# Kernel optimization log

Measured on AMD Instinct MI355X. Metric: run time of the kernel, lower is better.

Reference implementation:

```python
import jax, jax.numpy as jnp
import numpy as np

HUGE = 1e8  # stand-in for ops.HUGE_INT

B, P, Q, PD, QD = 16, 1024, 512, 768, 768


def setup_inputs() -> dict:
    key = jax.random.key(0)
    k1, k2, k3, k4, k5 = jax.random.split(key, 5)
    p = jax.random.normal(k1, (B, P, PD), dtype=jnp.float32)
    q = jax.random.normal(k2, (B, Q, QD), dtype=jnp.float32)
    # True = padded position (masked out before softmax)
    p_masks = jax.random.randint(k3, (B, P), 0, 2).astype(bool)
    q_masks = jax.random.randint(k4, (B, Q), 0, 2).astype(bool)
    # projection weight of Linear(q_dim, p_dim, bias=False): [p_dim, q_dim]
    W = jax.random.normal(k5, (PD, QD), dtype=jnp.float32) / np.sqrt(QD)
    return {"p": p, "q": q, "p_masks": p_masks, "q_masks": q_masks, "W": W}


def reference(p, q, p_masks, q_masks, W):
    # q_proj = project(q): [B,Q,p_dim]; dropout=0.0 -> identity
    q_proj = jnp.einsum('bqd,pd->bqp', q, W)
    # affinity = p @ q_proj^T : [B,P,Q]
    affinity = jnp.einsum('bpd,bqd->bpq', p, q_proj)
    # normalize over dim 1 with padding mask broadcast over last dim
    attn_over_p = jax.nn.softmax(
        jnp.where(p_masks[:, :, None], -HUGE, affinity), axis=1)  # [B,P,Q]
    attn_over_q = jax.nn.softmax(
        jnp.where(q_masks[:, :, None], -HUGE, jnp.swapaxes(affinity, 1, 2)), axis=1)  # [B,Q,P]
    # attn(weights[B,W2,W3], cand[B,W2,C3]) -> [B,W3,C3] = weights^T @ cand
    q_to_p_attn_vec = jnp.einsum('bpq,bpd->bqd', attn_over_p, p)  # [B,Q,p_dim]
    cand = jnp.concatenate([q, q_to_p_attn_vec], axis=2)  # [B,Q,q_dim+p_dim]
    p_to_q_attn_vec = jnp.einsum('bqp,bqc->bpc', attn_over_q, cand)  # [B,P,q_dim+p_dim]
    return (p_to_q_attn_vec, q_to_p_attn_vec)
```

## Files before the change

### kernel.cpp

```cpp
#include <hip/hip_runtime.h>
#include <math.h>

constexpr int B_  = 16;
constexpr int P_  = 1024;
constexpr int Q_  = 512;
constexpr int PD_ = 768;
constexpr int QD_ = 768;
constexpr int CD_ = 1536;

#define HUGE_NEG (-1e8f)

typedef __attribute__((ext_vector_type(8))) _Float16 f16x8;
typedef __attribute__((ext_vector_type(4))) _Float16 f16x4;
typedef __attribute__((ext_vector_type(4))) float f32x4;

__device__ __forceinline__ void dma16(const void* g, void* l) {
  __builtin_amdgcn_global_load_lds((__attribute__((address_space(1))) void*)g,
                                   (__attribute__((address_space(3))) void*)l,
                                   16, 0, 0);
}

__global__ __launch_bounds__(256) void k_cvt(const float* __restrict__ src,
                                             _Float16* __restrict__ dst, int n8) {
  int i = blockIdx.x * 256 + threadIdx.x;
  if (i >= n8) return;
  float4 a = ((const float4*)src)[2 * i];
  float4 b = ((const float4*)src)[2 * i + 1];
  f16x8 o = {(_Float16)a.x, (_Float16)a.y, (_Float16)a.z, (_Float16)a.w,
             (_Float16)b.x, (_Float16)b.y, (_Float16)b.z, (_Float16)b.w};
  ((f16x8*)dst)[i] = o;
}

__global__ __launch_bounds__(256) void k_prep(const float* __restrict__ src,
                                              _Float16* __restrict__ dst16,
                                              _Float16* __restrict__ dstT,
                                              int R, int C, size_t tBatch) {
  __shared__ _Float16 T[64][72];
  int r0 = blockIdx.x * 64, c0 = blockIdx.y * 64, b = blockIdx.z;
  const float* S = src + (size_t)b * R * C;
  _Float16* D16 = dst16 + (size_t)b * R * C;
  int tid = threadIdx.x;
  int rr = tid >> 4;
  int cc = (tid & 15) * 4;
#pragma unroll
  for (int k = 0; k < 4; ++k) {
    int r = rr + k * 16;
    float4 v = *(const float4*)(S + (size_t)(r0 + r) * C + c0 + cc);
    f16x4 h = {(_Float16)v.x, (_Float16)v.y, (_Float16)v.z, (_Float16)v.w};
    *(f16x4*)(D16 + (size_t)(r0 + r) * C + c0 + cc) = h;
    T[cc + 0][r] = h[0];
    T[cc + 1][r] = h[1];
    T[cc + 2][r] = h[2];
    T[cc + 3][r] = h[3];
  }
  __syncthreads();
  int cr = tid >> 2;
  int rc = (tid & 3) * 16;
  _Float16* D = dstT + (size_t)b * tBatch + (size_t)(c0 + cr) * R + r0;
  *(f16x8*)(D + rc) = *(f16x8*)&T[cr][rc];
  *(f16x8*)(D + rc + 8) = *(f16x8*)&T[cr][rc + 8];
}

__global__ __launch_bounds__(256) void k_w(
    const float* __restrict__ aff, const int* __restrict__ pmask,
    const int* __restrict__ qmask, const float* __restrict__ rpm,
    const float* __restrict__ rps, const float* __restrict__ pmax_part,
    const float* __restrict__ psum_part, _Float16* __restrict__ WP,
    _Float16* __restrict__ WQ) {
  __shared__ _Float16 T[64][72];
  __shared__ float rmx[64], rin[64], cmx[64], cin[64];
  int p0 = blockIdx.x * 64, q0 = blockIdx.y * 64, b = blockIdx.z;
  int tid = threadIdx.x;
  if (tid < 64) {
    int pp = p0 + tid;
    float m = -INFINITY;
#pragma unroll
    for (int z = 0; z < 4; ++z) m = fmaxf(m, rpm[(b * 4 + z) * P_ + pp]);
    float s = 0.f;
#pragma unroll
    for (int z = 0; z < 4; ++z)
      s += rps[(b * 4 + z) * P_ + pp] * __expf(rpm[(b * 4 + z) * P_ + pp] - m);
    rmx[tid] = m;
    rin[tid] = 1.0f / s;
  } else if (tid < 128) {
    int t = tid - 64;
    int qq = q0 + t;
    float m = -INFINITY;
#pragma unroll
    for (int z = 0; z < 4; ++z) m = fmaxf(m, pmax_part[(b * 4 + z) * Q_ + qq]);
    float s = 0.f;
#pragma unroll
    for (int z = 0; z < 4; ++z)
      s += psum_part[(b * 4 + z) * Q_ + qq] *
           __expf(pmax_part[(b * 4 + z) * Q_ + qq] - m);
    cmx[t] = m;
    cin[t] = 1.0f / s;
  }
  __syncthreads();
  const float* A = aff + (size_t)b * P_ * Q_;
  const int* pm = pmask + b * P_;
  int rr = tid >> 4;
  int cc = (tid & 15) * 4;
  int4 qm4 = *(const int4*)(qmask + b * Q_ + q0 + cc);
  int qm[4] = {qm4.x, qm4.y, qm4.z, qm4.w};
#pragma unroll
  for (int k = 0; k < 4; ++k) {
    int r = rr + k * 16;
    int msk = pm[p0 + r];
    float4 v = *(const float4*)(A + (size_t)(p0 + r) * Q_ + q0 + cc);
    float vv[4] = {v.x, v.y, v.z, v.w};
    f16x4 wp;
#pragma unroll
    for (int j = 0; j < 4; ++j) {
      wp[j] = (_Float16)(__expf((qm[j] ? HUGE_NEG : vv[j]) - rmx[r]) * rin[r]);
      T[cc + j][r] =
          (_Float16)(__expf((msk ? HUGE_NEG : vv[j]) - cmx[cc + j]) * cin[cc + j]);
    }
    *(f16x4*)(WP + ((size_t)b * P_ + p0 + r) * Q_ + q0 + cc) = wp;
  }
  __syncthreads();
  int cr = tid >> 2;
  int rc = (tid & 3) * 16;
  _Float16* D = WQ + ((size_t)b * Q_ + q0 + cr) * P_ + p0;
  *(f16x8*)(D + rc) = *(f16x8*)&T[cr][rc];
  *(f16x8*)(D + rc + 8) = *(f16x8*)&T[cr][rc + 8];
}

template <int NT, int LDA, int LDB>
__device__ __forceinline__ void gemm_core(const _Float16* __restrict__ Ab,
                                          const _Float16* __restrict__ Bb,
                                          _Float16* As, _Float16* Bs,
                                          f32x4 (&acc)[4][4], int w, int l) {
  constexpr int ASZ = 256 * 32, BSZ = 128 * 32;
  int rA = w * 32 + (l >> 2);
  int rB = w * 16 + (l >> 2);
  int sk = ((l & 3) ^ ((l >> 3) & 3)) * 8;
  int fr = l & 15;
  int fsw = (((l >> 4) ^ ((fr >> 1) & 3))) * 8;
  int wr = w >> 1, wc = w & 1;

  auto stage = [&](int buf, int t) {
    const _Float16* ga = Ab + (size_t)rA * LDA + t * 32 + sk;
    const _Float16* gb = Bb + (size_t)rB * LDB + t * 32 + sk;
    _Float16* la = As + buf * ASZ + (w * 32) * 32;
    _Float16* lb = Bs + buf * BSZ + (w * 16) * 32;
    dma16(ga, la);
    dma16(ga + 16 * LDA, la + 16 * 32);
    dma16(gb, lb);
  };
  auto compute = [&](int buf) {
    const _Float16* A0 = As + buf * ASZ;
    const _Float16* B0 = Bs + buf * BSZ;
    f16x8 a[4];
#pragma unroll
    for (int m = 0; m < 4; ++m)
      a[m] = *(const f16x8*)(A0 + (wr * 64 + m * 16 + fr) * 32 + fsw);
#pragma unroll
    for (int n = 0; n < 4; ++n) {
      f16x8 bn = *(const f16x8*)(B0 + (wc * 64 + n * 16 + fr) * 32 + fsw);
#pragma unroll
      for (int m = 0; m < 4; ++m)
        acc[m][n] =
            __builtin_amdgcn_mfma_f32_16x16x32_f16(a[m], bn, acc[m][n], 0, 0, 0);
    }
  };

  stage(0, 0);
  stage(1, 1);
  int b0 = 0, b1 = 1, b2 = 2;
#pragma unroll 3
  for (int t = 0; t < NT - 2; ++t) {
    stage(b2, t + 2);
    asm volatile("s_waitcnt vmcnt(6)" ::: "memory");
    __builtin_amdgcn_s_barrier();
    __builtin_amdgcn_sched_barrier(0);
    compute(b0);
    __builtin_amdgcn_s_barrier();
    int tmp = b0; b0 = b1; b1 = b2; b2 = tmp;
  }
  asm volatile("s_waitcnt vmcnt(3)" ::: "memory");
  __builtin_amdgcn_s_barrier();
  __builtin_amdgcn_sched_barrier(0);
  compute(b0);
  __builtin_amdgcn_s_barrier();
  asm volatile("s_waitcnt vmcnt(0)" ::: "memory");
  __builtin_amdgcn_s_barrier();
  __builtin_amdgcn_sched_barrier(0);
  compute(b1);
}

#define SWZ_DECODE(GX, GY)                                          \
  int lin = blockIdx.x + (GX) * (blockIdx.y + (GY) * blockIdx.z);   \
  constexpr int NWG = (GX) * (GY) * B_;                             \
  int w8 = (lin & 7) * (NWG / 8) + (lin >> 3);                      \
  int j0 = (w8 % (GX)) * 128;                                       \
  int t_ = w8 / (GX);                                               \
  int i0 = (t_ % (GY)) * 256;                                       \
  int b = t_ / (GY);

__global__ __launch_bounds__(512, 4) void k1_proj(
    const _Float16* __restrict__ q16, const _Float16* __restrict__ W16,
    _Float16* __restrict__ qp) {
  __shared__ alignas(16) _Float16 As[3 * 256 * 32];
  __shared__ alignas(16) _Float16 Bs[3 * 128 * 32];
  SWZ_DECODE(PD_ / 128, Q_ / 256)
  int tid = threadIdx.x, w = tid >> 6, l = tid & 63;
  f32x4 acc[4][4];
#pragma unroll
  for (int m = 0; m < 4; ++m)
#pragma unroll
    for (int n = 0; n < 4; ++n) acc[m][n] = (f32x4){0.f, 0.f, 0.f, 0.f};
  gemm_core<QD_ / 32, QD_, QD_>(q16 + (size_t)b * Q_ * QD_ + (size_t)i0 * QD_,
                                W16 + (size_t)j0 * QD_, As, Bs, acc, w, l);
  int wr = w >> 1, wc = w & 1, fr = l & 15, fq = l >> 4;
  _Float16* O = qp + (size_t)b * Q_ * PD_;
#pragma unroll
  for (int m = 0; m < 4; ++m) {
    int rl = wr * 64 + m * 16 + fq * 4;
#pragma unroll
    for (int n = 0; n < 4; ++n) {
      int cl = wc * 64 + n * 16 + fr;
#pragma unroll
      for (int r = 0; r < 4; ++r)
        O[(size_t)(i0 + rl + r) * PD_ + j0 + cl] = (_Float16)acc[m][n][r];
    }
  }
}

__global__ __launch_bounds__(512, 4) void k2_aff(
    const _Float16* __restrict__ p16, const _Float16* __restrict__ qp,
    const int* __restrict__ pmask, const int* __restrict__ qmask,
    float* __restrict__ aff, float* __restrict__ pmax_part,
    float* __restrict__ psum_part, float* __restrict__ rpm,
    float* __restrict__ rps) {
  __shared__ alignas(16) _Float16 As[3 * 256 * 32];
  __shared__ alignas(16) _Float16 Bs[3 * 128 * 32];
  SWZ_DECODE(Q_ / 128, P_ / 256)
  int tid = threadIdx.x, w = tid >> 6, l = tid & 63;
  f32x4 acc[4][4];
#pragma unroll
  for (int m = 0; m < 4; ++m)
#pragma unroll
    for (int n = 0; n < 4; ++n) acc[m][n] = (f32x4){0.f, 0.f, 0.f, 0.f};
  gemm_core<PD_ / 32, PD_, PD_>(p16 + (size_t)b * P_ * PD_ + (size_t)i0 * PD_,
                                qp + (size_t)b * Q_ * PD_ + (size_t)j0 * PD_,
                                As, Bs, acc, w, l);
  int wr = w >> 1, wc = w & 1, fr = l & 15, fq = l >> 4;
  float* Cb = aff + (size_t)b * P_ * Q_;
#pragma unroll
  for (int m = 0; m < 4; ++m) {
    int rl = wr * 64 + m * 16 + fq * 4;
#pragma unroll
    for (int n = 0; n < 4; ++n) {
      int cl = wc * 64 + n * 16 + fr;
#pragma unroll
      for (int r = 0; r < 4; ++r)
        Cb[(size_t)(i0 + rl + r) * Q_ + j0 + cl] = acc[m][n][r];
    }
  }
  const int* pmb = pmask + b * P_ + i0;
  unsigned pmbits = 0;
#pragma unroll
  for (int m = 0; m < 4; ++m)
#pragma unroll
    for (int r = 0; r < 4; ++r)
      pmbits |= (pmb[wr * 64 + m * 16 + fq * 4 + r] ? 1u : 0u) << (m * 4 + r);
  int qmv[4];
  {
    const int* qmb = qmask + b * Q_ + j0 + wc * 64 + fr;
#pragma unroll
    for (int n = 0; n < 4; ++n) qmv[n] = qmb[n * 16];
  }
  __syncthreads();
  float* scr = (float*)As;
  float* cm_ = scr;
  float* cs_ = scr + 512;
  float* rm_ = scr + 1024;
  float* rs_ = scr + 1536;

#pragma unroll
  for (int n = 0; n < 4; ++n) {
    float ml = -1e30f;
#pragma unroll
    for (int m = 0; m < 4; ++m)
#pragma unroll
      for (int r = 0; r < 4; ++r) {
        float v = ((pmbits >> (m * 4 + r)) & 1) ? HUGE_NEG : acc[m][n][r];
        ml = fmaxf(ml, v);
      }
    float sl = 0.f;
#pragma unroll
    for (int m = 0; m < 4; ++m)
#pragma unroll
      for (int r = 0; r < 4; ++r) {
        float v = ((pmbits >> (m * 4 + r)) & 1) ? HUGE_NEG : acc[m][n][r];
        sl += __expf(v - ml);
      }
#pragma unroll
    for (int off = 16; off <= 32; off <<= 1) {
      float om = __shfl_xor(ml, off);
      float os = __shfl_xor(sl, off);
      float nm = fmaxf(ml, om);
      sl = sl * __expf(ml - nm) + os * __expf(om - nm);
      ml = nm;
    }
    if (fq == 0) {
      int col = wc * 64 + n * 16 + fr;
      cm_[wr * 128 + col] = ml;
      cs_[wr * 128 + col] = sl;
    }
  }
#pragma unroll
  for (int m = 0; m < 4; ++m)
#pragma unroll
    for (int r = 0; r < 4; ++r) {
      float ml = -1e30f;
#pragma unroll
      for (int n = 0; n < 4; ++n) {
        float v = qmv[n] ? HUGE_NEG : acc[m][n][r];
        ml = fmaxf(ml, v);
      }
      float sl = 0.f;
#pragma unroll
      for (int n = 0; n < 4; ++n) {
        float v = qmv[n] ? HUGE_NEG : acc[m][n][r];
        sl += __expf(v - ml);
      }
#pragma unroll
      for (int off = 1; off <= 8; off <<= 1) {
        float om = __shfl_xor(ml, off);
        float os = __shfl_xor(sl, off);
        float nm = fmaxf(ml, om);
        sl = sl * __expf(ml - nm) + os * __expf(om - nm);
        ml = nm;
      }
      if (fr == 0) {
        int row = wr * 64 + m * 16 + fq * 4 + r;
        rm_[wc * 256 + row] = ml;
        rs_[wc * 256 + row] = sl;
      }
    }
  __syncthreads();
  if (tid < 128) {
    float nm = fmaxf(fmaxf(cm_[tid], cm_[128 + tid]),
                     fmaxf(cm_[256 + tid], cm_[384 + tid]));
    float ns = cs_[tid] * __expf(cm_[tid] - nm) +
               cs_[128 + tid] * __expf(cm_[128 + tid] - nm) +
               cs_[256 + tid] * __expf(cm_[256 + tid] - nm) +
               cs_[384 + tid] * __expf(cm_[384 + tid] - nm);
    int z = i0 >> 8;
    pmax_part[(b * 4 + z) * Q_ + j0 + tid] = nm;
    psum_part[(b * 4 + z) * Q_ + j0 + tid] = ns;
  } else if (tid >= 256) {
    int t = tid - 256;
    float m0 = rm_[t], m1 = rm_[256 + t];
    float s0 = rs_[t], s1 = rs_[256 + t];
    float nm = fmaxf(m0, m1);
    float ns = s0 * __expf(m0 - nm) + s1 * __expf(m1 - nm);
    int zj = j0 >> 7;
    rpm[(b * 4 + zj) * P_ + i0 + t] = nm;
    rps[(b * 4 + zj) * P_ + i0 + t] = ns;
  }
}

__global__ __launch_bounds__(512, 4) void k4_attn(
    const _Float16* __restrict__ WQ, const _Float16* __restrict__ pT,
    float* __restrict__ out2, _Float16* __restrict__ candT) {
  __shared__ alignas(16) _Float16 As[3 * 256 * 32];
  __shared__ alignas(16) _Float16 Bs[3 * 128 * 32];
  SWZ_DECODE(PD_ / 128, Q_ / 256)
  int tid = threadIdx.x, w = tid >> 6, l = tid & 63;
  f32x4 acc[4][4];
#pragma unroll
  for (int m = 0; m < 4; ++m)
#pragma unroll
    for (int n = 0; n < 4; ++n) acc[m][n] = (f32x4){0.f, 0.f, 0.f, 0.f};
  gemm_core<P_ / 32, P_, P_>(WQ + (size_t)b * Q_ * P_ + (size_t)i0 * P_,
                             pT + (size_t)b * PD_ * P_ + (size_t)j0 * P_, As,
                             Bs, acc, w, l);
  int wr = w >> 1, wc = w & 1, fr = l & 15, fq = l >> 4;
  float* Cb = out2 + (size_t)b * Q_ * PD_;
  _Float16* Tb = candT + (size_t)b * CD_ * Q_;
#pragma unroll
  for (int m = 0; m < 4; ++m) {
    int rl = wr * 64 + m * 16 + fq * 4;
#pragma unroll
    for (int n = 0; n < 4; ++n) {
      int cl = wc * 64 + n * 16 + fr;
      f16x4 cv;
#pragma unroll
      for (int r = 0; r < 4; ++r) {
        float v = acc[m][n][r];
        Cb[(size_t)(i0 + rl + r) * PD_ + j0 + cl] = v;
        cv[r] = (_Float16)v;
      }
      *(f16x4*)(Tb + (size_t)(QD_ + j0 + cl) * Q_ + i0 + rl) = cv;
    }
  }
}

__global__ __launch_bounds__(512, 4) void k5_attn(
    const _Float16* __restrict__ WP, const _Float16* __restrict__ candT,
    float* __restrict__ out1) {
  __shared__ alignas(16) _Float16 As[3 * 256 * 32];
  __shared__ alignas(16) _Float16 Bs[3 * 128 * 32];
  SWZ_DECODE(CD_ / 128, P_ / 256)
  int tid = threadIdx.x, w = tid >> 6, l = tid & 63;
  f32x4 acc[4][4];
#pragma unroll
  for (int m = 0; m < 4; ++m)
#pragma unroll
    for (int n = 0; n < 4; ++n) acc[m][n] = (f32x4){0.f, 0.f, 0.f, 0.f};
  gemm_core<Q_ / 32, Q_, Q_>(WP + (size_t)b * P_ * Q_ + (size_t)i0 * Q_,
                             candT + (size_t)b * CD_ * Q_ + (size_t)j0 * Q_, As,
                             Bs, acc, w, l);
  int wr = w >> 1, wc = w & 1, fr = l & 15, fq = l >> 4;
  float* Cb = out1 + (size_t)b * P_ * CD_;
#pragma unroll
  for (int m = 0; m < 4; ++m) {
    int rl = wr * 64 + m * 16 + fq * 4;
#pragma unroll
    for (int n = 0; n < 4; ++n) {
      int cl = wc * 64 + n * 16 + fr;
#pragma unroll
      for (int r = 0; r < 4; ++r)
        Cb[(size_t)(i0 + rl + r) * CD_ + j0 + cl] = acc[m][n][r];
    }
  }
}

extern "C" void kernel_launch(void* const* d_in, const int* in_sizes, int n_in,
                              void* d_out, int out_size, void* d_ws,
                              size_t ws_size, hipStream_t stream) {
  const float* p = (const float*)d_in[0];
  const float* q = (const float*)d_in[1];
  const int* pmask = (const int*)d_in[2];
  const int* qmask = (const int*)d_in[3];
  const float* W = (const float*)d_in[4];
  float* out = (float*)d_out;

  char* ws = (char*)d_ws;
  size_t off = 0;
  auto alloc = [&](size_t bytes) {
    void* r = ws + off;
    off += (bytes + 255) & ~(size_t)255;
    return r;
  };
  _Float16* q16 = (_Float16*)alloc((size_t)B_ * Q_ * QD_ * 2);
  _Float16* p16 = (_Float16*)alloc((size_t)B_ * P_ * PD_ * 2);
  _Float16* pT = (_Float16*)alloc((size_t)B_ * PD_ * P_ * 2);
  _Float16* candT = (_Float16*)alloc((size_t)B_ * CD_ * Q_ * 2);
  _Float16* W16 = (_Float16*)alloc((size_t)PD_ * QD_ * 2);
  _Float16* qp16 = (_Float16*)alloc((size_t)B_ * Q_ * PD_ * 2);
  float* aff = (float*)alloc((size_t)B_ * P_ * Q_ * 4);
  _Float16* WP = (_Float16*)alloc((size_t)B_ * P_ * Q_ * 2);
  _Float16* WQ = (_Float16*)alloc((size_t)B_ * Q_ * P_ * 2);
  float* pmax_part = (float*)alloc((size_t)B_ * 4 * Q_ * 4);
  float* psum_part = (float*)alloc((size_t)B_ * 4 * Q_ * 4);
  float* rpm = (float*)alloc((size_t)B_ * 4 * P_ * 4);
  float* rps = (float*)alloc((size_t)B_ * 4 * P_ * 4);

  float* out1 = out;
  float* out2 = out + (size_t)B_ * P_ * CD_;

  k_cvt<<<PD_ * QD_ / 8 / 256, 256, 0, stream>>>(W, W16, PD_ * QD_ / 8);
  k_prep<<<dim3(Q_ / 64, QD_ / 64, B_), 256, 0, stream>>>(
      q, q16, candT, Q_, QD_, (size_t)CD_ * Q_);
  k_prep<<<dim3(P_ / 64, PD_ / 64, B_), 256, 0, stream>>>(
      p, p16, pT, P_, PD_, (size_t)PD_ * P_);
  k1_proj<<<dim3(PD_ / 128, Q_ / 256, B_), 512, 0, stream>>>(q16, W16, qp16);
  k2_aff<<<dim3(Q_ / 128, P_ / 256, B_), 512, 0, stream>>>(
      p16, qp16, pmask, qmask, aff, pmax_part, psum_part, rpm, rps);
  k_w<<<dim3(P_ / 64, Q_ / 64, B_), 256, 0, stream>>>(
      aff, pmask, qmask, rpm, rps, pmax_part, psum_part, WP, WQ);
  k4_attn<<<dim3(PD_ / 128, Q_ / 256, B_), 512, 0, stream>>>(WQ, pT, out2,
                                                             candT);
  k5_attn<<<dim3(CD_ / 128, P_ / 256, B_), 512, 0, stream>>>(WP, candT, out1);
}
```

Baseline: 168.0 us.

## Compact unmasked rows and shrink softmax-weighted GEMM K loops by valid count

Adds a per-batch index kernel that stream-compacts the unmasked positions of p and q to the front, and permutes the intermediate layouts (pT, candT, qproj, WQ) into that compacted order. The two attention GEMMs then run their K loop only over the padded count of valid positions, skipping the roughly half of the reduction that masked positions contribute as exact zeros after softmax. Masks in the affinity and weight kernels are rebuilt from the compacted counts. The cost is extra index kernels, gathered loads, separate conversion passes for p and q instead of the fused convert-and-transpose, and scattered output writes. Correctness depends on masked rows having zero weight and on the permutations lining up across kernels.

Result: no change. 168.7 us (+0.5%).

```diff
diff --git a/kernel.cpp b/kernel.cpp
--- a/kernel.cpp
+++ b/kernel.cpp
@@ -18,6 +18,50 @@
   __builtin_amdgcn_global_load_lds((__attribute__((address_space(1))) void*)g,
                                    (__attribute__((address_space(3))) void*)l,
                                    16, 0, 0);
+}
+
+__global__ __launch_bounds__(256) void k_index(const int* __restrict__ mask,
+                                               int N, int* __restrict__ idx,
+                                               int* __restrict__ cnt,
+                                               int* __restrict__ nt) {
+  int b = blockIdx.x;
+  const int* mb = mask + b * N;
+  int* ib = idx + b * N;
+  int tid = threadIdx.x;
+  int w = tid >> 6, lane = tid & 63;
+  int nch = N / 64;
+  __shared__ int ccnt[16];
+  __shared__ int coff[17];
+  for (int c = w; c < nch; c += 4) {
+    bool un = (mb[c * 64 + lane] == 0);
+    unsigned long long bal = __ballot(un);
+    if (lane == 0) ccnt[c] = __popcll(bal);
+  }
+  __syncthreads();
+  if (tid == 0) {
+    int s = 0;
+    for (int c = 0; c < nch; ++c) {
+      coff[c] = s;
+      s += ccnt[c];
+    }
+    coff[nch] = s;
+    cnt[b] = s;
+    int c32 = (s + 31) & ~31;
+    if (c32 < 64) c32 = 64;
+    nt[b] = c32 / 32;
+  }
+  __syncthreads();
+  int total = coff[nch];
+  for (int c = w; c < nch; c += 4) {
+    int e = c * 64 + lane;
+    bool un = (mb[e] == 0);
+    unsigned long long bal = __ballot(un);
+    int pre = __popcll(bal & ((1ull << lane) - 1ull));
+    if (un)
+      ib[coff[c] + pre] = e;
+    else
+      ib[total + (c * 64 - coff[c]) + (lane - pre)] = e;
+  }
 }
 
 __global__ __launch_bounds__(256) void k_cvt(const float* __restrict__ src,
@@ -31,23 +75,24 @@
   ((f16x8*)dst)[i] = o;
 }
 
-__global__ __launch_bounds__(256) void k_prep(const float* __restrict__ src,
-                                              _Float16* __restrict__ dst16,
-                                              _Float16* __restrict__ dstT,
-                                              int R, int C, size_t tBatch) {
+__global__ __launch_bounds__(256) void k_gprep(const _Float16* __restrict__ src,
+                                               const int* __restrict__ idx,
+                                               _Float16* __restrict__ dstT,
+                                               int R, int C, size_t tBatch,
+                                               int colOff) {
   __shared__ _Float16 T[64][72];
+  __shared__ int sIdx[64];
   int r0 = blockIdx.x * 64, c0 = blockIdx.y * 64, b = blockIdx.z;
-  const float* S = src + (size_t)b * R * C;
-  _Float16* D16 = dst16 + (size_t)b * R * C;
   int tid = threadIdx.x;
+  if (tid < 64) sIdx[tid] = idx[b * R + r0 + tid];
+  __syncthreads();
+  const _Float16* S = src + (size_t)b * R * C;
   int rr = tid >> 4;
   int cc = (tid & 15) * 4;
 #pragma unroll
   for (int k = 0; k < 4; ++k) {
     int r = rr + k * 16;
-    float4 v = *(const float4*)(S + (size_t)(r0 + r) * C + c0 + cc);
-    f16x4 h = {(_Float16)v.x, (_Float16)v.y, (_Float16)v.z, (_Float16)v.w};
-    *(f16x4*)(D16 + (size_t)(r0 + r) * C + c0 + cc) = h;
+    f16x4 h = *(const f16x4*)(S + (size_t)sIdx[r] * C + c0 + cc);
     T[cc + 0][r] = h[0];
     T[cc + 1][r] = h[1];
     T[cc + 2][r] = h[2];
@@ -56,30 +101,33 @@
   __syncthreads();
   int cr = tid >> 2;
   int rc = (tid & 3) * 16;
-  _Float16* D = dstT + (size_t)b * tBatch + (size_t)(c0 + cr) * R + r0;
+  _Float16* D = dstT + (size_t)b * tBatch + (size_t)(colOff + c0 + cr) * R + r0;
   *(f16x8*)(D + rc) = *(f16x8*)&T[cr][rc];
   *(f16x8*)(D + rc + 8) = *(f16x8*)&T[cr][rc + 8];
 }
 
 __global__ __launch_bounds__(256) void k_w(
-    const float* __restrict__ aff, const int* __restrict__ pmask,
-    const int* __restrict__ qmask, const float* __restrict__ rpm,
-    const float* __restrict__ rps, const float* __restrict__ pmax_part,
-    const float* __restrict__ psum_part, _Float16* __restrict__ WP,
-    _Float16* __restrict__ WQ) {
+    const float* __restrict__ aff, const int* __restrict__ idxP_,
+    const int* __restrict__ cntP_, const int* __restrict__ cntQ_,
+    const float* __restrict__ rpm, const float* __restrict__ rps,
+    const float* __restrict__ pmax_part, const float* __restrict__ psum_part,
+    _Float16* __restrict__ WP, _Float16* __restrict__ WQ) {
   __shared__ _Float16 T[64][72];
   __shared__ float rmx[64], rin[64], cmx[64], cin[64];
-  int p0 = blockIdx.x * 64, q0 = blockIdx.y * 64, b = blockIdx.z;
+  __shared__ int sIdx[64];
+  int s0 = blockIdx.x * 64, q0 = blockIdx.y * 64, b = blockIdx.z;
   int tid = threadIdx.x;
+  int cntP = cntP_[b], cntQ = cntQ_[b];
   if (tid < 64) {
-    int pp = p0 + tid;
+    int op = idxP_[b * P_ + s0 + tid];
+    sIdx[tid] = op;
     float m = -INFINITY;
 #pragma unroll
-    for (int z = 0; z < 4; ++z) m = fmaxf(m, rpm[(b * 4 + z) * P_ + pp]);
+    for (int z = 0; z < 4; ++z) m = fmaxf(m, rpm[(b * 4 + z) * P_ + op]);
     float s = 0.f;
 #pragma unroll
     for (int z = 0; z < 4; ++z)
-      s += rps[(b * 4 + z) * P_ + pp] * __expf(rpm[(b * 4 + z) * P_ + pp] - m);
+      s += rps[(b * 4 + z) * P_ + op] * __expf(rpm[(b * 4 + z) * P_ + op] - m);
     rmx[tid] = m;
     rin[tid] = 1.0f / s;
   } else if (tid < 128) {
@@ -98,16 +146,17 @@
   }
   __syncthreads();
   const float* A = aff + (size_t)b * P_ * Q_;
-  const int* pm = pmask + b * P_;
   int rr = tid >> 4;
   int cc = (tid & 15) * 4;
-  int4 qm4 = *(const int4*)(qmask + b * Q_ + q0 + cc);
-  int qm[4] = {qm4.x, qm4.y, qm4.z, qm4.w};
+  int qm[4];
+#pragma unroll
+  for (int j = 0; j < 4; ++j) qm[j] = (q0 + cc + j >= cntQ);
 #pragma unroll
   for (int k = 0; k < 4; ++k) {
     int r = rr + k * 16;
-    int msk = pm[p0 + r];
-    float4 v = *(const float4*)(A + (size_t)(p0 + r) * Q_ + q0 + cc);
+    int orig = sIdx[r];
+    int msk = (s0 + r >= cntP);
+    float4 v = *(const float4*)(A + (size_t)orig * Q_ + q0 + cc);
     float vv[4] = {v.x, v.y, v.z, v.w};
     f16x4 wp;
 #pragma unroll
@@ -116,37 +165,32 @@
       T[cc + j][r] =
           (_Float16)(__expf((msk ? HUGE_NEG : vv[j]) - cmx[cc + j]) * cin[cc + j]);
     }
-    *(f16x4*)(WP + ((size_t)b * P_ + p0 + r) * Q_ + q0 + cc) = wp;
+    *(f16x4*)(WP + ((size_t)b * P_ + orig) * Q_ + q0 + cc) = wp;
   }
   __syncthreads();
   int cr = tid >> 2;
   int rc = (tid & 3) * 16;
-  _Float16* D = WQ + ((size_t)b * Q_ + q0 + cr) * P_ + p0;
+  _Float16* D = WQ + ((size_t)b * Q_ + q0 + cr) * P_ + s0;
   *(f16x8*)(D + rc) = *(f16x8*)&T[cr][rc];
   *(f16x8*)(D + rc + 8) = *(f16x8*)&T[cr][rc + 8];
 }
 
-template <int NT, int LDA, int LDB>
-__device__ __forceinline__ void gemm_core(const _Float16* __restrict__ Ab,
-                                          const _Float16* __restrict__ Bb,
-                                          _Float16* As, _Float16* Bs,
-                                          f32x4 (&acc)[4][4], int w, int l) {
+__device__ __forceinline__ void gemm_core(const _Float16* pA0,
+                                          const _Float16* pA1,
+                                          const _Float16* pB0, _Float16* As,
+                                          _Float16* Bs, f32x4 (&acc)[4][4],
+                                          int w, int l, int NT) {
   constexpr int ASZ = 256 * 32, BSZ = 128 * 32;
-  int rA = w * 32 + (l >> 2);
-  int rB = w * 16 + (l >> 2);
-  int sk = ((l & 3) ^ ((l >> 3) & 3)) * 8;
   int fr = l & 15;
   int fsw = (((l >> 4) ^ ((fr >> 1) & 3))) * 8;
   int wr = w >> 1, wc = w & 1;
 
   auto stage = [&](int buf, int t) {
-    const _Float16* ga = Ab + (size_t)rA * LDA + t * 32 + sk;
-    const _Float16* gb = Bb + (size_t)rB * LDB + t * 32 + sk;
     _Float16* la = As + buf * ASZ + (w * 32) * 32;
     _Float16* lb = Bs + buf * BSZ + (w * 16) * 32;
-    dma16(ga, la);
-    dma16(ga + 16 * LDA, la + 16 * 32);
-    dma16(gb, lb);
+    dma16(pA0 + t * 32, la);
+    dma16(pA1 + t * 32, la + 16 * 32);
+    dma16(pB0 + t * 32, lb);
   };
   auto compute = [&](int buf) {
     const _Float16* A0 = As + buf * ASZ;
@@ -189,6 +233,11 @@
   compute(b1);
 }
 
+#define LANE_BASES()                          \
+  int rA = w * 32 + (l >> 2);                 \
+  int rB = w * 16 + (l >> 2);                 \
+  int sk = ((l & 3) ^ ((l >> 3) & 3)) * 8;
+
 #define SWZ_DECODE(GX, GY)                                          \
   int lin = blockIdx.x + (GX) * (blockIdx.y + (GY) * blockIdx.z);   \
   constexpr int NWG = (GX) * (GY) * B_;                             \
@@ -200,18 +249,22 @@
 
 __global__ __launch_bounds__(512, 4) void k1_proj(
     const _Float16* __restrict__ q16, const _Float16* __restrict__ W16,
-    _Float16* __restrict__ qp) {
+    const int* __restrict__ idxQ, _Float16* __restrict__ qp) {
   __shared__ alignas(16) _Float16 As[3 * 256 * 32];
   __shared__ alignas(16) _Float16 Bs[3 * 128 * 32];
   SWZ_DECODE(PD_ / 128, Q_ / 256)
   int tid = threadIdx.x, w = tid >> 6, l = tid & 63;
+  LANE_BASES()
+  const _Float16* qb = q16 + (size_t)b * Q_ * QD_;
+  int o0 = idxQ[b * Q_ + i0 + rA];
+  int o1 = idxQ[b * Q_ + i0 + rA + 16];
   f32x4 acc[4][4];
 #pragma unroll
   for (int m = 0; m < 4; ++m)
 #pragma unroll
     for (int n = 0; n < 4; ++n) acc[m][n] = (f32x4){0.f, 0.f, 0.f, 0.f};
-  gemm_core<QD_ / 32, QD_, QD_>(q16 + (size_t)b * Q_ * QD_ + (size_t)i0 * QD_,
-                                W16 + (size_t)j0 * QD_, As, Bs, acc, w, l);
+  gemm_core(qb + (size_t)o0 * QD_ + sk, qb + (size_t)o1 * QD_ + sk,
+            W16 + (size_t)(j0 + rB) * QD_ + sk, As, Bs, acc, w, l, QD_ / 32);
   int wr = w >> 1, wc = w & 1, fr = l & 15, fq = l >> 4;
   _Float16* O = qp + (size_t)b * Q_ * PD_;
 #pragma unroll
@@ -229,7 +282,7 @@
 
 __global__ __launch_bounds__(512, 4) void k2_aff(
     const _Float16* __restrict__ p16, const _Float16* __restrict__ qp,
-    const int* __restrict__ pmask, const int* __restrict__ qmask,
+    const int* __restrict__ pmask, const int* __restrict__ cntQ_,
     float* __restrict__ aff, float* __restrict__ pmax_part,
     float* __restrict__ psum_part, float* __restrict__ rpm,
     float* __restrict__ rps) {
@@ -237,14 +290,17 @@
   __shared__ alignas(16) _Float16 Bs[3 * 128 * 32];
   SWZ_DECODE(Q_ / 128, P_ / 256)
   int tid = threadIdx.x, w = tid >> 6, l = tid & 63;
+  LANE_BASES()
+  const _Float16* pb = p16 + (size_t)b * P_ * PD_;
+  const _Float16* qpb = qp + (size_t)b * Q_ * PD_;
   f32x4 acc[4][4];
 #pragma unroll
   for (int m = 0; m < 4; ++m)
 #pragma unroll
     for (int n = 0; n < 4; ++n) acc[m][n] = (f32x4){0.f, 0.f, 0.f, 0.f};
-  gemm_core<PD_ / 32, PD_, PD_>(p16 + (size_t)b * P_ * PD_ + (size_t)i0 * PD_,
-                                qp + (size_t)b * Q_ * PD_ + (size_t)j0 * PD_,
-                                As, Bs, acc, w, l);
+  gemm_core(pb + (size_t)(i0 + rA) * PD_ + sk,
+            pb + (size_t)(i0 + rA + 16) * PD_ + sk,
+            qpb + (size_t)(j0 + rB) * PD_ + sk, As, Bs, acc, w, l, PD_ / 32);
   int wr = w >> 1, wc = w & 1, fr = l & 15, fq = l >> 4;
   float* Cb = aff + (size_t)b * P_ * Q_;
 #pragma unroll
@@ -265,11 +321,12 @@
 #pragma unroll
     for (int r = 0; r < 4; ++r)
       pmbits |= (pmb[wr * 64 + m * 16 + fq * 4 + r] ? 1u : 0u) << (m * 4 + r);
+  int cQ = cntQ_[b];
   int qmv[4];
   {
-    const int* qmb = qmask + b * Q_ + j0 + wc * 64 + fr;
-#pragma unroll
-    for (int n = 0; n < 4; ++n) qmv[n] = qmb[n * 16];
+    int cbase = j0 + wc * 64 + fr;
+#pragma unroll
+    for (int n = 0; n < 4; ++n) qmv[n] = (cbase + n * 16) >= cQ;
   }
   __syncthreads();
   float* scr = (float*)As;
@@ -364,26 +421,35 @@
 }
 
 __global__ __launch_bounds__(512, 4) void k4_attn(
-    const _Float16* __restrict__ WQ, const _Float16* __restrict__ pT,
+    const _Float16* __restrict__ WQ, const _Float16* __restrict__ pTc,
+    const int* __restrict__ idxQ, const int* __restrict__ ntP_,
     float* __restrict__ out2, _Float16* __restrict__ candT) {
   __shared__ alignas(16) _Float16 As[3 * 256 * 32];
   __shared__ alignas(16) _Float16 Bs[3 * 128 * 32];
   SWZ_DECODE(PD_ / 128, Q_ / 256)
   int tid = threadIdx.x, w = tid >> 6, l = tid & 63;
+  LANE_BASES()
+  const _Float16* Ab = WQ + (size_t)b * Q_ * P_;
+  const _Float16* Bb = pTc + (size_t)b * PD_ * P_;
+  int NT = ntP_[b];
   f32x4 acc[4][4];
 #pragma unroll
   for (int m = 0; m < 4; ++m)
 #pragma unroll
     for (int n = 0; n < 4; ++n) acc[m][n] = (f32x4){0.f, 0.f, 0.f, 0.f};
-  gemm_core<P_ / 32, P_, P_>(WQ + (size_t)b * Q_ * P_ + (size_t)i0 * P_,
-                             pT + (size_t)b * PD_ * P_ + (size_t)j0 * P_, As,
-                             Bs, acc, w, l);
+  gemm_core(Ab + (size_t)(i0 + rA) * P_ + sk,
+            Ab + (size_t)(i0 + rA + 16) * P_ + sk,
+            Bb + (size_t)(j0 + rB) * P_ + sk, As, Bs, acc, w, l, NT);
   int wr = w >> 1, wc = w & 1, fr = l & 15, fq = l >> 4;
   float* Cb = out2 + (size_t)b * Q_ * PD_;
   _Float16* Tb = candT + (size_t)b * CD_ * Q_;
+  const int* iq = idxQ + b * Q_;
 #pragma unroll
   for (int m = 0; m < 4; ++m) {
     int rl = wr * 64 + m * 16 + fq * 4;
+    int oq[4];
+#pragma unroll
+    for (int r = 0; r < 4; ++r) oq[r] = iq[i0 + rl + r];
 #pragma unroll
     for (int n = 0; n < 4; ++n) {
       int cl = wc * 64 + n * 16 + fr;
@@ -391,7 +457,7 @@
 #pragma unroll
       for (int r = 0; r < 4; ++r) {
         float v = acc[m][n][r];
-        Cb[(size_t)(i0 + rl + r) * PD_ + j0 + cl] = v;
+        Cb[(size_t)oq[r] * PD_ + j0 + cl] = v;
         cv[r] = (_Float16)v;
       }
       *(f16x4*)(Tb + (size_t)(QD_ + j0 + cl) * Q_ + i0 + rl) = cv;
@@ -401,19 +467,23 @@
 
 __global__ __launch_bounds__(512, 4) void k5_attn(
     const _Float16* __restrict__ WP, const _Float16* __restrict__ candT,
-    float* __restrict__ out1) {
+    const int* __restrict__ ntQ_, float* __restrict__ out1) {
   __shared__ alignas(16) _Float16 As[3 * 256 * 32];
   __shared__ alignas(16) _Float16 Bs[3 * 128 * 32];
   SWZ_DECODE(CD_ / 128, P_ / 256)
   int tid = threadIdx.x, w = tid >> 6, l = tid & 63;
+  LANE_BASES()
+  const _Float16* Ab = WP + (size_t)b * P_ * Q_;
+  const _Float16* Bb = candT + (size_t)b * CD_ * Q_;
+  int NT = ntQ_[b];
   f32x4 acc[4][4];
 #pragma unroll
   for (int m = 0; m < 4; ++m)
 #pragma unroll
     for (int n = 0; n < 4; ++n) acc[m][n] = (f32x4){0.f, 0.f, 0.f, 0.f};
-  gemm_core<Q_ / 32, Q_, Q_>(WP + (size_t)b * P_ * Q_ + (size_t)i0 * Q_,
-                             candT + (size_t)b * CD_ * Q_ + (size_t)j0 * Q_, As,
-                             Bs, acc, w, l);
+  gemm_core(Ab + (size_t)(i0 + rA) * Q_ + sk,
+            Ab + (size_t)(i0 + rA + 16) * Q_ + sk,
+            Bb + (size_t)(j0 + rB) * Q_ + sk, As, Bs, acc, w, l, NT);
   int wr = w >> 1, wc = w & 1, fr = l & 15, fq = l >> 4;
   float* Cb = out1 + (size_t)b * P_ * CD_;
 #pragma unroll
@@ -448,7 +518,7 @@
   };
   _Float16* q16 = (_Float16*)alloc((size_t)B_ * Q_ * QD_ * 2);
   _Float16* p16 = (_Float16*)alloc((size_t)B_ * P_ * PD_ * 2);
-  _Float16* pT = (_Float16*)alloc((size_t)B_ * PD_ * P_ * 2);
+  _Float16* pTc = (_Float16*)alloc((size_t)B_ * PD_ * P_ * 2);
   _Float16* candT = (_Float16*)alloc((size_t)B_ * CD_ * Q_ * 2);
   _Float16* W16 = (_Float16*)alloc((size_t)PD_ * QD_ * 2);
   _Float16* qp16 = (_Float16*)alloc((size_t)B_ * Q_ * PD_ * 2);
@@ -459,21 +529,33 @@
   float* psum_part = (float*)alloc((size_t)B_ * 4 * Q_ * 4);
   float* rpm = (float*)alloc((size_t)B_ * 4 * P_ * 4);
   float* rps = (float*)alloc((size_t)B_ * 4 * P_ * 4);
+  int* idxP = (int*)alloc((size_t)B_ * P_ * 4);
+  int* idxQ = (int*)alloc((size_t)B_ * Q_ * 4);
+  int* cntP = (int*)alloc(B_ * 4);
+  int* cntQ = (int*)alloc(B_ * 4);
+  int* ntP = (int*)alloc(B_ * 4);
+  int* ntQ = (int*)alloc(B_ * 4);
 
   float* out1 = out;
   float* out2 = out + (size_t)B_ * P_ * CD_;
 
+  k_index<<<B_, 256, 0, stream>>>(pmask, P_, idxP, cntP, ntP);
+  k_index<<<B_, 256, 0, stream>>>(qmask, Q_, idxQ, cntQ, ntQ);
   k_cvt<<<PD_ * QD_ / 8 / 256, 256, 0, stream>>>(W, W16, PD_ * QD_ / 8);
-  k_prep<<<dim3(Q_ / 64, QD_ / 64, B_), 256, 0, stream>>>(
-      q, q16, candT, Q_, QD_, (size_t)CD_ * Q_);
-  k_prep<<<dim3(P_ / 64, PD_ / 64, B_), 256, 0, stream>>>(
-      p, p16, pT, P_, PD_, (size_t)PD_ * P_);
-  k1_proj<<<dim3(PD_ / 128, Q_ / 256, B_), 512, 0, stream>>>(q16, W16, qp16);
+  k_cvt<<<B_ * Q_ * QD_ / 8 / 256, 256, 0, stream>>>(q, q16, B_ * Q_ * QD_ / 8);
+  k_cvt<<<B_ * P_ * PD_ / 8 / 256, 256, 0, stream>>>(p, p16, B_ * P_ * PD_ / 8);
+  k_gprep<<<dim3(Q_ / 64, QD_ / 64, B_), 256, 0, stream>>>(
+      q16, idxQ, candT, Q_, QD_, (size_t)CD_ * Q_, 0);
+  k_gprep<<<dim3(P_ / 64, PD_ / 64, B_), 256, 0, stream>>>(
+      p16, idxP, pTc, P_, PD_, (size_t)PD_ * P_, 0);
+  k1_proj<<<dim3(PD_ / 128, Q_ / 256, B_), 512, 0, stream>>>(q16, W16, idxQ,
+                                                             qp16);
   k2_aff<<<dim3(Q_ / 128, P_ / 256, B_), 512, 0, stream>>>(
-      p16, qp16, pmask, qmask, aff, pmax_part, psum_part, rpm, rps);
+      p16, qp16, pmask, cntQ, aff, pmax_part, psum_part, rpm, rps);
   k_w<<<dim3(P_ / 64, Q_ / 64, B_), 256, 0, stream>>>(
-      aff, pmask, qmask, rpm, rps, pmax_part, psum_part, WP, WQ);
-  k4_attn<<<dim3(PD_ / 128, Q_ / 256, B_), 512, 0, stream>>>(WQ, pT, out2,
-                                                             candT);
-  k5_attn<<<dim3(CD_ / 128, P_ / 256, B_), 512, 0, stream>>>(WP, candT, out1);
-}
+      aff, idxP, cntP, cntQ, rpm, rps, pmax_part, psum_part, WP, WQ);
+  k4_attn<<<dim3(PD_ / 128, Q_ / 256, B_), 512, 0, stream>>>(WQ, pTc, idxQ,
+                                                             ntP, out2, candT);
+  k5_attn<<<dim3(CD_ / 128, P_ / 256, B_), 512, 0, stream>>>(WP, candT, ntQ,
+                                                             out1);
+}
```
